# Optimization experiments

Hardware: AMD Instinct MI355X
Metric: run time of the kernel (lower is better)

Reference implementation:

```python
import jax, jax.numpy as jnp
import numpy as np

B, S, D, O, E = 8, 4096, 1024, 1024, 64

def setup_inputs() -> dict:
    key = jax.random.key(0)
    kx, kgw, kgb, kew, keb = jax.random.split(key, 5)
    x = jax.random.normal(kx, (B, S, D), dtype=jnp.float32)
    gate_w = jax.random.normal(kgw, (E, D), dtype=jnp.float32) * 0.02
    gate_b = jnp.zeros((E,), dtype=jnp.float32)
    expert_w = jax.random.normal(kew, (E, D, O), dtype=jnp.float32) * 0.02
    expert_b = jnp.zeros((E, O), dtype=jnp.float32)
    return {"x": x, "gate_w": gate_w, "gate_b": gate_b,
            "expert_w": expert_w, "expert_b": expert_b}

def reference(x, gate_w, gate_b, expert_w, expert_b):
    # x: [B,S,D] -> flatten tokens. With world_size=1 the all-reduce and
    # all-to-alls in the torch module are identities, and per-chunk processing
    # is token-independent, so one global pass is mathematically identical.
    b, s, d = x.shape
    xt = x.reshape(-1, d)                                   # [N, D]
    logits = xt @ gate_w.T + gate_b                         # [N, E]
    gates = jax.nn.softmax(logits, axis=-1)
    sel = jnp.argmax(gates, axis=-1)                        # [N] top-1 expert
    order = jnp.argsort(sel)                                # stable sort by expert
    xs = xt[order]                                          # tokens grouped by expert
    counts = jnp.bincount(sel, length=E).astype(jnp.int32)  # tokens per expert
    # Grouped expert GEMM: row block e of xs multiplies expert_w[e].
    ys = jax.lax.ragged_dot(xs, expert_w, counts)           # [N, O]
    ys = ys + expert_b[sel[order]]
    # Combine: scatter sorted outputs back to original token positions.
    # (Note: torch output is NOT scaled by gate probability.)
    out = jnp.zeros((xt.shape[0], expert_w.shape[-1]), dtype=ys.dtype)
    out = out.at[order].set(ys)
    return out.reshape(b, s, -1)
```

## Files before the change

### kernel.cpp

```cpp
#include <hip/hip_runtime.h>
#include <hip/hip_bf16.h>

#define N_TOK 32768
#define DIM 1024
#define OUTD 1024
#define NEXP 64

typedef __attribute__((ext_vector_type(4))) float f32x4;
typedef __attribute__((ext_vector_type(8))) short bf16x8;

__device__ __forceinline__ unsigned short f2bf(float f) {
    unsigned int u = __builtin_bit_cast(unsigned int, f);
    u += 0x7FFFu + ((u >> 16) & 1u);
    return (unsigned short)(u >> 16);
}

#define GLOAD16(gp, lp) \
    __builtin_amdgcn_global_load_lds((const __attribute__((address_space(1))) void*)(gp), \
                                     (__attribute__((address_space(3))) void*)(lp), 16, 0, 0)

__global__ __launch_bounds__(256) void prep_kernel(const float* __restrict__ x,
        const float* __restrict__ gw, const float* __restrict__ gb,
        const float* __restrict__ ew,
        int* __restrict__ sel, int* __restrict__ nflag, int* __restrict__ flags,
        unsigned short* __restrict__ xb, unsigned short* __restrict__ wt)
{
    __shared__ __align__(16) char smem[18432];
    int tid = threadIdx.x;

    if (blockIdx.x < 512) {
        float (*xs)[36]  = (float(*)[36])smem;
        float (*wsm)[36] = (float(*)[36])(smem + 9216);
        int t0 = blockIdx.x * 64;
        int tg = tid >> 4, eg = tid & 15;

        float acc[4][4];
#pragma unroll
        for (int i = 0; i < 4; i++)
#pragma unroll
            for (int j = 0; j < 4; j++) acc[i][j] = 0.f;

        for (int k0 = 0; k0 < DIM; k0 += 32) {
            __syncthreads();
#pragma unroll
            for (int q = 0; q < 2; q++) {
                int cidx = tid + q * 256;
                int r = cidx >> 3, c4 = (cidx & 7) * 4;
                *reinterpret_cast<float4*>(&xs[r][c4]) =
                    *reinterpret_cast<const float4*>(&x[(size_t)(t0 + r) * DIM + k0 + c4]);
                *reinterpret_cast<float4*>(&wsm[r][c4]) =
                    *reinterpret_cast<const float4*>(&gw[(size_t)r * DIM + k0 + c4]);
            }
            __syncthreads();
            if (xb) {
                int r = tid >> 2, cc = (tid & 3) * 8;
                float4 v0 = *reinterpret_cast<const float4*>(&xs[r][cc]);
                float4 v1 = *reinterpret_cast<const float4*>(&xs[r][cc + 4]);
                uint4 p;
                p.x = (unsigned int)f2bf(v0.x) | ((unsigned int)f2bf(v0.y) << 16);
                p.y = (unsigned int)f2bf(v0.z) | ((unsigned int)f2bf(v0.w) << 16);
                p.z = (unsigned int)f2bf(v1.x) | ((unsigned int)f2bf(v1.y) << 16);
                p.w = (unsigned int)f2bf(v1.z) | ((unsigned int)f2bf(v1.w) << 16);
                *reinterpret_cast<uint4*>(&xb[(size_t)(t0 + r) * DIM + k0 + cc]) = p;
            }
#pragma unroll
            for (int kk4 = 0; kk4 < 8; kk4++) {
                float4 xv[4], wv[4];
#pragma unroll
                for (int i = 0; i < 4; i++)
                    xv[i] = *reinterpret_cast<const float4*>(&xs[tg + 16 * i][kk4 * 4]);
#pragma unroll
                for (int j = 0; j < 4; j++)
                    wv[j] = *reinterpret_cast<const float4*>(&wsm[eg + 16 * j][kk4 * 4]);
#pragma unroll
                for (int i = 0; i < 4; i++)
#pragma unroll
                    for (int j = 0; j < 4; j++) {
                        acc[i][j] = fmaf(xv[i].x, wv[j].x, acc[i][j]);
                        acc[i][j] = fmaf(xv[i].y, wv[j].y, acc[i][j]);
                        acc[i][j] = fmaf(xv[i].z, wv[j].z, acc[i][j]);
                        acc[i][j] = fmaf(xv[i].w, wv[j].w, acc[i][j]);
                    }
            }
        }
#pragma unroll
        for (int j = 0; j < 4; j++) {
            float b = gb[eg + 16 * j];
#pragma unroll
            for (int i = 0; i < 4; i++) acc[i][j] += b;
        }
#pragma unroll
        for (int i = 0; i < 4; i++) {
            float m1 = -1e30f, m2 = -1e30f; int e1 = 0;
#pragma unroll
            for (int j = 0; j < 4; j++) {
                float v = acc[i][j]; int e = eg + 16 * j;
                if (v > m1) { m2 = m1; m1 = v; e1 = e; }
                else if (v > m2) m2 = v;
            }
#pragma unroll
            for (int d = 1; d < 16; d <<= 1) {
                float om1 = __shfl_xor(m1, d, 16);
                float om2 = __shfl_xor(m2, d, 16);
                int   oe1 = __shfl_xor(e1, d, 16);
                if (om1 > m1 || (om1 == m1 && oe1 < e1)) {
                    m2 = fmaxf(om2, m1); m1 = om1; e1 = oe1;
                } else {
                    m2 = fmaxf(m2, om1);
                }
            }
            if (eg == 0) {
                int t = t0 + tg + 16 * i;
                sel[t] = e1;
                if (m1 - m2 < 1e-3f) {
                    int idx = atomicAdd(nflag, 1);
                    if (idx < 4096) flags[idx] = t;
                }
            }
        }
    } else {
        if (!wt) return;
        unsigned short (*ts)[68] = (unsigned short(*)[68])smem;
        int lin = blockIdx.x - 512;
        int e = lin >> 8;
        int d0 = (lin & 15) * 64, o0 = ((lin >> 4) & 15) * 64;
        const float* src = ew + (size_t)e * (DIM * OUTD);
        int r = tid >> 4, c = (tid & 15) * 4;
#pragma unroll
        for (int i = 0; i < 4; i++) {
            int rr = r + i * 16;
            float4 v = *reinterpret_cast<const float4*>(&src[(size_t)(d0 + rr) * OUTD + o0 + c]);
            ushort4 u;
            u.x = f2bf(v.x); u.y = f2bf(v.y); u.z = f2bf(v.z); u.w = f2bf(v.w);
            *reinterpret_cast<ushort4*>(&ts[rr][c]) = u;
        }
        __syncthreads();
        unsigned short* dst = wt + (size_t)e * (DIM * OUTD);
        int dc = tid & 7;
#pragma unroll
        for (int i = 0; i < 2; i++) {
            int oo = (tid >> 3) + i * 32;
            uint4 p;
            p.x = (unsigned int)ts[dc*8+0][oo] | ((unsigned int)ts[dc*8+1][oo] << 16);
            p.y = (unsigned int)ts[dc*8+2][oo] | ((unsigned int)ts[dc*8+3][oo] << 16);
            p.z = (unsigned int)ts[dc*8+4][oo] | ((unsigned int)ts[dc*8+5][oo] << 16);
            p.w = (unsigned int)ts[dc*8+6][oo] | ((unsigned int)ts[dc*8+7][oo] << 16);
            *reinterpret_cast<uint4*>(&dst[(size_t)(o0 + oo) * DIM + d0 + dc * 8]) = p;
        }
    }
}

__global__ __launch_bounds__(64) void gate_fix_kernel(const float* __restrict__ x,
        const float* __restrict__ gw, const float* __restrict__ gb,
        int* __restrict__ sel, const int* __restrict__ nflag, const int* __restrict__ flags)
{
    int n = *nflag; if (n > 4096) n = 4096;
    int b = blockIdx.x;
    if (b >= n) return;
    int t = flags[b];
    int e = threadIdx.x;
    const float* xr = x + (size_t)t * DIM;
    const float* wr = gw + (size_t)e * DIM;
    double acc = (double)gb[e];
    for (int k = 0; k < DIM; k += 4) {
        acc += (double)xr[k]   * (double)wr[k];
        acc += (double)xr[k+1] * (double)wr[k+1];
        acc += (double)xr[k+2] * (double)wr[k+2];
        acc += (double)xr[k+3] * (double)wr[k+3];
    }
    double m1 = acc; int e1 = e;
#pragma unroll
    for (int d = 1; d < 64; d <<= 1) {
        double om1 = __shfl_xor(m1, d, 64);
        int   oe1  = __shfl_xor(e1, d, 64);
        if (om1 > m1 || (om1 == m1 && oe1 < e1)) { m1 = om1; e1 = oe1; }
    }
    if (e == 0) sel[t] = e1;
}

__global__ __launch_bounds__(256) void hist_kernel(const int* __restrict__ sel,
                                                   int* __restrict__ counts)
{
    __shared__ int h[NEXP];
    int tid = threadIdx.x;
    if (tid < NEXP) h[tid] = 0;
    __syncthreads();
    int t = blockIdx.x * 256 + tid;
    atomicAdd(&h[sel[t]], 1);
    __syncthreads();
    if (tid < NEXP && h[tid]) atomicAdd(&counts[tid], h[tid]);
}

__global__ void sched_kernel(const int* __restrict__ counts, int* __restrict__ offsets,
                             int* __restrict__ schedE, int* __restrict__ schedR,
                             int* __restrict__ totalRB)
{
    if (threadIdx.x != 0) return;
    int off = 0, rb = 0;
    for (int e = 0; e < NEXP; e++) {
        int c = counts[e];
        offsets[e] = off;
        int nb = (c + 127) >> 7;
        for (int b2 = 0; b2 < nb; b2++) { schedE[rb] = e; schedR[rb] = b2 * 128; rb++; }
        off += c;
    }
    offsets[NEXP] = off;
    *totalRB = rb;
}

__global__ __launch_bounds__(256) void scatter_kernel(const int* __restrict__ sel,
        const int* __restrict__ offsets, int* __restrict__ cursor, int* __restrict__ perm)
{
    int t = blockIdx.x * 256 + threadIdx.x;
    int e = sel[t];
    int pos = offsets[e] + atomicAdd(&cursor[e], 1);
    perm[pos] = t;
}

__global__ __launch_bounds__(256) void moe_gemm2(
        const unsigned short* __restrict__ xb, const unsigned short* __restrict__ wt,
        const float* __restrict__ eb,
        const int* __restrict__ perm, const int* __restrict__ offsets,
        const int* __restrict__ counts, const int* __restrict__ schedE,
        const int* __restrict__ schedR, const int* __restrict__ totalRB,
        float* __restrict__ out)
{
    int lin = blockIdx.x;
    int rb = lin >> 3, cb = lin & 7;
    if (rb >= *totalRB) return;
    int e = schedE[rb], r0 = schedR[rb];
    int cnt = counts[e], base = offsets[e];

    __shared__ __align__(16) unsigned short As[8192];
    __shared__ __align__(16) unsigned short Bs[8192];
    __shared__ int toks[128];

    int tid = threadIdx.x;
    if (tid < 128) {
        int r = r0 + tid;
        toks[tid] = (r < cnt) ? perm[base + r] : -1;
    }
    __syncthreads();

    int lane = tid & 63;
    int wv = tid >> 6;
    int wr = wv >> 1, wc = wv & 1;
    int lr = lane & 15, lg = lane >> 4;

    int rowS = tid >> 2;
    int koff = (((tid & 3) ^ ((tid >> 3) & 3)) * 8);
    int tokA1 = toks[rowS];      if (tokA1 < 0) tokA1 = 0;
    int tokA2 = toks[64 + rowS]; if (tokA2 < 0) tokA2 = 0;

    const unsigned short* wte = wt + ((size_t)e << 20);
    const unsigned short* bSrc1 = wte + (size_t)(cb * 128 + rowS) * DIM + koff;
    const unsigned short* bSrc2 = wte + (size_t)(cb * 128 + 64 + rowS) * DIM + koff;
    const unsigned short* aSrc1 = xb + (size_t)tokA1 * DIM + koff;
    const unsigned short* aSrc2 = xb + (size_t)tokA2 * DIM + koff;

    unsigned short* AsW0 = As + wv * 512;
    unsigned short* AsW1 = As + 2048 + wv * 512;
    unsigned short* BsW0 = Bs + wv * 512;
    unsigned short* BsW1 = Bs + 2048 + wv * 512;

    f32x4 acc[4][4];
#pragma unroll
    for (int m = 0; m < 4; m++)
#pragma unroll
        for (int n = 0; n < 4; n++)
#pragma unroll
            for (int c = 0; c < 4; c++) acc[m][n][c] = 0.f;

    const char* Asc = (const char*)As;
    const char* Bsc = (const char*)Bs;
    int fko = ((lg ^ ((lr >> 1) & 3)) * 16);

    auto stage = [&](int buf, int k0) {
        int off = buf * 4096;
        GLOAD16(bSrc1 + k0, BsW0 + off);
        GLOAD16(bSrc2 + k0, BsW1 + off);
        GLOAD16(aSrc1 + k0, AsW0 + off);
        GLOAD16(aSrc2 + k0, AsW1 + off);
    };
    auto compute = [&](int buf) {
        int boff = buf * 8192;
        bf16x8 bfr[4];
#pragma unroll
        for (int n = 0; n < 4; n++) {
            int row = wc * 64 + n * 16 + lr;
            bfr[n] = *reinterpret_cast<const bf16x8*>(Bsc + boff + (row << 6) + fko);
        }
#pragma unroll
        for (int m = 0; m < 4; m++) {
            int row = wr * 64 + m * 16 + lr;
            bf16x8 afr = *reinterpret_cast<const bf16x8*>(Asc + boff + (row << 6) + fko);
#pragma unroll
            for (int n = 0; n < 4; n++)
                acc[m][n] = __builtin_amdgcn_mfma_f32_16x16x32_bf16(afr, bfr[n], acc[m][n], 0, 0, 0);
        }
    };

    stage(0, 0);
    asm volatile("s_waitcnt vmcnt(0)" ::: "memory");
    __builtin_amdgcn_s_barrier();
    asm volatile("" ::: "memory");

    int cur = 0;
#pragma unroll 1
    for (int t = 0; t < 31; ++t) {
        stage(cur ^ 1, (t + 1) * 32);
        compute(cur);
        asm volatile("s_waitcnt vmcnt(0)" ::: "memory");
        __builtin_amdgcn_s_barrier();
        asm volatile("" ::: "memory");
        cur ^= 1;
    }
    compute(cur);

#pragma unroll
    for (int n = 0; n < 4; n++) {
        int oc = cb * 128 + wc * 64 + n * 16 + lr;
        float bias = eb[e * OUTD + oc];
#pragma unroll
        for (int m = 0; m < 4; m++) {
#pragma unroll
            for (int i2 = 0; i2 < 4; i2++) {
                int rr = wr * 64 + m * 16 + lg * 4 + i2;
                int tk = toks[rr];
                if (tk >= 0)
                    out[(size_t)tk * OUTD + oc] = acc[m][n][i2] + bias;
            }
        }
    }
}

__global__ __launch_bounds__(256) void moe_gemm_legacy(const float* __restrict__ x,
        const float* __restrict__ ew, const float* __restrict__ eb,
        const int* __restrict__ perm, const int* __restrict__ offsets,
        const int* __restrict__ counts, const int* __restrict__ schedE,
        const int* __restrict__ schedR, const int* __restrict__ totalRB,
        float* __restrict__ out)
{
    int rb = blockIdx.x;
    if (rb >= *totalRB) return;
    int cb = blockIdx.y;
    int e = schedE[rb], r0 = schedR[rb];
    int cnt = counts[e], base = offsets[e];

    __shared__ __align__(16) unsigned short As[128][40];
    __shared__ __align__(16) unsigned short Bs[128][40];
    __shared__ int toks[128];

    int tid = threadIdx.x;
    if (tid < 128) {
        int r = r0 + tid;
        toks[tid] = (r < cnt) ? perm[base + r] : -1;
    }
    __syncthreads();

    int lane = tid & 63;
    int wave = tid >> 6;
    int wr = wave >> 1, wc = wave & 1;
    int lr = lane & 15, lg = lane >> 4;

    f32x4 acc[4][4];
#pragma unroll
    for (int m = 0; m < 4; m++)
#pragma unroll
        for (int n = 0; n < 4; n++)
#pragma unroll
            for (int c = 0; c < 4; c++) acc[m][n][c] = 0.f;

    int aRow[4]; int aTok[4];
#pragma unroll
    for (int q = 0; q < 4; q++) {
        aRow[q] = (tid >> 3) + q * 32;
        int tk = toks[aRow[q]];
        aTok[q] = (tk < 0) ? 0 : tk;
    }
    int ac4 = tid & 7;
    int d0 = (tid >> 5) * 4;
    int o_lane = tid & 31;
    const float* wb = ew + (size_t)e * (DIM * OUTD) + (size_t)cb * 128;

    for (int k0 = 0; k0 < DIM; k0 += 32) {
        float4 av[4];
#pragma unroll
        for (int q = 0; q < 4; q++)
            av[q] = *reinterpret_cast<const float4*>(&x[(size_t)aTok[q] * DIM + k0 + ac4 * 4]);
        float bv[4][4];
#pragma unroll
        for (int i2 = 0; i2 < 4; i2++)
#pragma unroll
            for (int j = 0; j < 4; j++)
                bv[i2][j] = wb[(size_t)(k0 + d0 + i2) * OUTD + o_lane + 32 * j];

        __syncthreads();
#pragma unroll
        for (int q = 0; q < 4; q++) {
            uint2 p;
            p.x = (unsigned int)f2bf(av[q].x) | ((unsigned int)f2bf(av[q].y) << 16);
            p.y = (unsigned int)f2bf(av[q].z) | ((unsigned int)f2bf(av[q].w) << 16);
            *reinterpret_cast<uint2*>(&As[aRow[q]][ac4 * 4]) = p;
        }
#pragma unroll
        for (int j = 0; j < 4; j++) {
            uint2 p;
            p.x = (unsigned int)f2bf(bv[0][j]) | ((unsigned int)f2bf(bv[1][j]) << 16);
            p.y = (unsigned int)f2bf(bv[2][j]) | ((unsigned int)f2bf(bv[3][j]) << 16);
            *reinterpret_cast<uint2*>(&Bs[o_lane + 32 * j][d0]) = p;
        }
        __syncthreads();

        bf16x8 bfr[4];
#pragma unroll
        for (int n = 0; n < 4; n++)
            bfr[n] = *reinterpret_cast<const bf16x8*>(&Bs[wc * 64 + n * 16 + lr][lg * 8]);
#pragma unroll
        for (int m = 0; m < 4; m++) {
            bf16x8 afr = *reinterpret_cast<const bf16x8*>(&As[wr * 64 + m * 16 + lr][lg * 8]);
#pragma unroll
            for (int n = 0; n < 4; n++)
                acc[m][n] = __builtin_amdgcn_mfma_f32_16x16x32_bf16(afr, bfr[n], acc[m][n], 0, 0, 0);
        }
    }

#pragma unroll
    for (int n = 0; n < 4; n++) {
        int oc = cb * 128 + wc * 64 + n * 16 + lr;
        float bias = eb[e * OUTD + oc];
#pragma unroll
        for (int m = 0; m < 4; m++) {
#pragma unroll
            for (int i2 = 0; i2 < 4; i2++) {
                int rr = wr * 64 + m * 16 + lg * 4 + i2;
                int tk = toks[rr];
                if (tk >= 0)
                    out[(size_t)tk * OUTD + oc] = acc[m][n][i2] + bias;
            }
        }
    }
}

extern "C" void kernel_launch(void* const* d_in, const int* in_sizes, int n_in,
                              void* d_out, int out_size, void* d_ws, size_t ws_size,
                              hipStream_t stream)
{
    const float* x  = (const float*)d_in[0];
    const float* gw = (const float*)d_in[1];
    const float* gb = (const float*)d_in[2];
    const float* ew = (const float*)d_in[3];
    const float* eb = (const float*)d_in[4];
    float* out = (float*)d_out;

    char* ws = (char*)d_ws;
    int* counts  = (int*)(ws + 0);
    int* cursor  = (int*)(ws + 256);
    int* offsets = (int*)(ws + 512);
    int* totalRB = (int*)(ws + 1024);
    int* nflag   = (int*)(ws + 1028);
    int* flags   = (int*)(ws + 1032);
    int* schedE  = (int*)(ws + 20480);
    int* schedR  = (int*)(ws + 22528);
    int* sel     = (int*)(ws + 24576);
    int* perm    = (int*)(ws + 155648);

    const size_t WT_OFF   = (size_t)1 << 20;
    const size_t WT_BYTES = (size_t)NEXP * DIM * OUTD * 2;
    const size_t XB_OFF   = WT_OFF + WT_BYTES;
    const size_t XB_BYTES = (size_t)N_TOK * DIM * 2;
    int mode = (ws_size >= XB_OFF + XB_BYTES) ? 2
             : (ws_size >= WT_OFF + WT_BYTES) ? 1 : 0;
    unsigned short* wt = (mode >= 1) ? (unsigned short*)(ws + WT_OFF) : nullptr;
    unsigned short* xb = (mode == 2) ? (unsigned short*)(ws + XB_OFF) : nullptr;

    hipMemsetAsync(ws, 0, 2048, stream);

    prep_kernel<<<dim3(512 + ((mode >= 1) ? 16384 : 0)), 256, 0, stream>>>(
        x, gw, gb, ew, sel, nflag, flags, xb, wt);
    gate_fix_kernel<<<dim3(4096), 64, 0, stream>>>(x, gw, gb, sel, nflag, flags);
    hist_kernel<<<dim3(N_TOK / 256), 256, 0, stream>>>(sel, counts);
    sched_kernel<<<dim3(1), 64, 0, stream>>>(counts, offsets, schedE, schedR, totalRB);
    scatter_kernel<<<dim3(N_TOK / 256), 256, 0, stream>>>(sel, offsets, cursor, perm);

    if (mode == 2)
        moe_gemm2<<<dim3(2560), 256, 0, stream>>>(xb, wt, eb, perm, offsets, counts,
                                                  schedE, schedR, totalRB, out);
    else
        moe_gemm_legacy<<<dim3(320, 8), 256, 0, stream>>>(x, ew, eb, perm, offsets, counts,
                                                          schedE, schedR, totalRB, out);
}
```

Baseline: 445.8 us.

## Enlarge expert GEMM tile to 256x256, fuse histogram into gating, parallelize scheduling

The grouped expert GEMM moves from 128x128 tiles with 256 threads to 256x256 tiles with 512 threads (8 waves, 128x64 per wave). It also gets an XCD-aware block-to-tile mapping, so each weight and activation tile is reused across more MFMA work. The separate histogram kernel is removed: per-expert counts are now gathered with global atomics in the gating kernel and patched in gate_fix when a near-tie token changes expert. The single-thread scheduler becomes a wave-wide prefix scan. The cost is a larger accumulator footprint with register-pressure risk under launch_bounds(512,2), more padding waste on partial row blocks, and contended global atomics on 64 counters.

```diff
diff --git a/kernel.cpp b/kernel.cpp
--- a/kernel.cpp
+++ b/kernel.cpp
@@ -23,6 +23,7 @@
         const float* __restrict__ gw, const float* __restrict__ gb,
         const float* __restrict__ ew,
         int* __restrict__ sel, int* __restrict__ nflag, int* __restrict__ flags,
+        int* __restrict__ counts,
         unsigned short* __restrict__ xb, unsigned short* __restrict__ wt)
 {
     __shared__ __align__(16) char smem[18432];
@@ -112,6 +113,7 @@
             if (eg == 0) {
                 int t = t0 + tg + 16 * i;
                 sel[t] = e1;
+                atomicAdd(&counts[e1], 1);
                 if (m1 - m2 < 1e-3f) {
                     int idx = atomicAdd(nflag, 1);
                     if (idx < 4096) flags[idx] = t;
@@ -152,7 +154,8 @@
 
 __global__ __launch_bounds__(64) void gate_fix_kernel(const float* __restrict__ x,
         const float* __restrict__ gw, const float* __restrict__ gb,
-        int* __restrict__ sel, const int* __restrict__ nflag, const int* __restrict__ flags)
+        int* __restrict__ sel, const int* __restrict__ nflag, const int* __restrict__ flags,
+        int* __restrict__ counts)
 {
     int n = *nflag; if (n > 4096) n = 4096;
     int b = blockIdx.x;
@@ -175,37 +178,35 @@
         int   oe1  = __shfl_xor(e1, d, 64);
         if (om1 > m1 || (om1 == m1 && oe1 < e1)) { m1 = om1; e1 = oe1; }
     }
-    if (e == 0) sel[t] = e1;
-}
-
-__global__ __launch_bounds__(256) void hist_kernel(const int* __restrict__ sel,
-                                                   int* __restrict__ counts)
-{
-    __shared__ int h[NEXP];
-    int tid = threadIdx.x;
-    if (tid < NEXP) h[tid] = 0;
-    __syncthreads();
-    int t = blockIdx.x * 256 + tid;
-    atomicAdd(&h[sel[t]], 1);
-    __syncthreads();
-    if (tid < NEXP && h[tid]) atomicAdd(&counts[tid], h[tid]);
+    if (e == 0) {
+        int eOld = sel[t];
+        if (eOld != e1) {
+            sel[t] = e1;
+            atomicSub(&counts[eOld], 1);
+            atomicAdd(&counts[e1], 1);
+        }
+    }
 }
 
 __global__ void sched_kernel(const int* __restrict__ counts, int* __restrict__ offsets,
                              int* __restrict__ schedE, int* __restrict__ schedR,
-                             int* __restrict__ totalRB)
-{
-    if (threadIdx.x != 0) return;
-    int off = 0, rb = 0;
-    for (int e = 0; e < NEXP; e++) {
-        int c = counts[e];
-        offsets[e] = off;
-        int nb = (c + 127) >> 7;
-        for (int b2 = 0; b2 < nb; b2++) { schedE[rb] = e; schedR[rb] = b2 * 128; rb++; }
-        off += c;
-    }
-    offsets[NEXP] = off;
-    *totalRB = rb;
+                             int* __restrict__ totalRB, int rowsShift)
+{
+    int e = threadIdx.x;
+    int c = counts[e];
+    int v = c;
+#pragma unroll
+    for (int d = 1; d < 64; d <<= 1) { int y = __shfl_up(v, d, 64); if (e >= d) v += y; }
+    offsets[e] = v - c;
+    if (e == 63) offsets[NEXP] = v;
+    int rows = 1 << rowsShift;
+    int nb = (c + rows - 1) >> rowsShift;
+    int rbv = nb;
+#pragma unroll
+    for (int d = 1; d < 64; d <<= 1) { int y = __shfl_up(rbv, d, 64); if (e >= d) rbv += y; }
+    int rbBase = rbv - nb;
+    for (int i = 0; i < nb; i++) { schedE[rbBase + i] = e; schedR[rbBase + i] = i << rowsShift; }
+    if (e == 63) *totalRB = rbv;
 }
 
 __global__ __launch_bounds__(256) void scatter_kernel(const int* __restrict__ sel,
@@ -217,7 +218,7 @@
     perm[pos] = t;
 }
 
-__global__ __launch_bounds__(256) void moe_gemm2(
+__global__ __launch_bounds__(512, 2) void moe_gemm3(
         const unsigned short* __restrict__ xb, const unsigned short* __restrict__ wt,
         const float* __restrict__ eb,
         const int* __restrict__ perm, const int* __restrict__ offsets,
@@ -225,18 +226,20 @@
         const int* __restrict__ schedR, const int* __restrict__ totalRB,
         float* __restrict__ out)
 {
-    int lin = blockIdx.x;
-    int rb = lin >> 3, cb = lin & 7;
+    int xcd = blockIdx.x & 7;
+    int slot = blockIdx.x >> 3;
+    int rb = slot * 2 + (xcd >> 2);
+    int cb = xcd & 3;
     if (rb >= *totalRB) return;
     int e = schedE[rb], r0 = schedR[rb];
     int cnt = counts[e], base = offsets[e];
 
-    __shared__ __align__(16) unsigned short As[8192];
-    __shared__ __align__(16) unsigned short Bs[8192];
-    __shared__ int toks[128];
+    __shared__ __align__(16) unsigned short As[16384];
+    __shared__ __align__(16) unsigned short Bs[16384];
+    __shared__ int toks[256];
 
     int tid = threadIdx.x;
-    if (tid < 128) {
+    if (tid < 256) {
         int r = r0 + tid;
         toks[tid] = (r < cnt) ? perm[base + r] : -1;
     }
@@ -244,28 +247,28 @@
 
     int lane = tid & 63;
     int wv = tid >> 6;
-    int wr = wv >> 1, wc = wv & 1;
+    int wr = wv >> 2, wc = wv & 3;
     int lr = lane & 15, lg = lane >> 4;
 
     int rowS = tid >> 2;
-    int koff = (((tid & 3) ^ ((tid >> 3) & 3)) * 8);
-    int tokA1 = toks[rowS];      if (tokA1 < 0) tokA1 = 0;
-    int tokA2 = toks[64 + rowS]; if (tokA2 < 0) tokA2 = 0;
+    int koff = ((tid & 3) ^ ((tid >> 3) & 3)) * 8;
+    int tokA1 = toks[rowS];       if (tokA1 < 0) tokA1 = 0;
+    int tokA2 = toks[128 + rowS]; if (tokA2 < 0) tokA2 = 0;
 
     const unsigned short* wte = wt + ((size_t)e << 20);
-    const unsigned short* bSrc1 = wte + (size_t)(cb * 128 + rowS) * DIM + koff;
-    const unsigned short* bSrc2 = wte + (size_t)(cb * 128 + 64 + rowS) * DIM + koff;
     const unsigned short* aSrc1 = xb + (size_t)tokA1 * DIM + koff;
     const unsigned short* aSrc2 = xb + (size_t)tokA2 * DIM + koff;
-
-    unsigned short* AsW0 = As + wv * 512;
-    unsigned short* AsW1 = As + 2048 + wv * 512;
-    unsigned short* BsW0 = Bs + wv * 512;
-    unsigned short* BsW1 = Bs + 2048 + wv * 512;
-
-    f32x4 acc[4][4];
-#pragma unroll
-    for (int m = 0; m < 4; m++)
+    const unsigned short* bSrc1 = wte + (size_t)(cb * 256 + rowS) * DIM + koff;
+    const unsigned short* bSrc2 = wte + (size_t)(cb * 256 + 128 + rowS) * DIM + koff;
+
+    unsigned short* AsQ0 = As + wv * 512;
+    unsigned short* AsQ1 = As + 4096 + wv * 512;
+    unsigned short* BsQ0 = Bs + wv * 512;
+    unsigned short* BsQ1 = Bs + 4096 + wv * 512;
+
+    f32x4 acc[8][4];
+#pragma unroll
+    for (int m = 0; m < 8; m++)
 #pragma unroll
         for (int n = 0; n < 4; n++)
 #pragma unroll
@@ -273,17 +276,17 @@
 
     const char* Asc = (const char*)As;
     const char* Bsc = (const char*)Bs;
-    int fko = ((lg ^ ((lr >> 1) & 3)) * 16);
+    int fko = (lg ^ ((lr >> 1) & 3)) * 16;
 
     auto stage = [&](int buf, int k0) {
-        int off = buf * 4096;
-        GLOAD16(bSrc1 + k0, BsW0 + off);
-        GLOAD16(bSrc2 + k0, BsW1 + off);
-        GLOAD16(aSrc1 + k0, AsW0 + off);
-        GLOAD16(aSrc2 + k0, AsW1 + off);
+        int off = buf * 8192;
+        GLOAD16(bSrc1 + k0, BsQ0 + off);
+        GLOAD16(bSrc2 + k0, BsQ1 + off);
+        GLOAD16(aSrc1 + k0, AsQ0 + off);
+        GLOAD16(aSrc2 + k0, AsQ1 + off);
     };
     auto compute = [&](int buf) {
-        int boff = buf * 8192;
+        int boff = buf * 16384;
         bf16x8 bfr[4];
 #pragma unroll
         for (int n = 0; n < 4; n++) {
@@ -291,8 +294,8 @@
             bfr[n] = *reinterpret_cast<const bf16x8*>(Bsc + boff + (row << 6) + fko);
         }
 #pragma unroll
-        for (int m = 0; m < 4; m++) {
-            int row = wr * 64 + m * 16 + lr;
+        for (int m = 0; m < 8; m++) {
+            int row = wr * 128 + m * 16 + lr;
             bf16x8 afr = *reinterpret_cast<const bf16x8*>(Asc + boff + (row << 6) + fko);
 #pragma unroll
             for (int n = 0; n < 4; n++)
@@ -319,13 +322,13 @@
 
 #pragma unroll
     for (int n = 0; n < 4; n++) {
-        int oc = cb * 128 + wc * 64 + n * 16 + lr;
+        int oc = cb * 256 + wc * 64 + n * 16 + lr;
         float bias = eb[e * OUTD + oc];
 #pragma unroll
-        for (int m = 0; m < 4; m++) {
+        for (int m = 0; m < 8; m++) {
 #pragma unroll
             for (int i2 = 0; i2 < 4; i2++) {
-                int rr = wr * 64 + m * 16 + lg * 4 + i2;
+                int rr = wr * 128 + m * 16 + lg * 4 + i2;
                 int tk = toks[rr];
                 if (tk >= 0)
                     out[(size_t)tk * OUTD + oc] = acc[m][n][i2] + bias;
@@ -469,23 +472,22 @@
     const size_t WT_BYTES = (size_t)NEXP * DIM * OUTD * 2;
     const size_t XB_OFF   = WT_OFF + WT_BYTES;
     const size_t XB_BYTES = (size_t)N_TOK * DIM * 2;
-    int mode = (ws_size >= XB_OFF + XB_BYTES) ? 2
-             : (ws_size >= WT_OFF + WT_BYTES) ? 1 : 0;
-    unsigned short* wt = (mode >= 1) ? (unsigned short*)(ws + WT_OFF) : nullptr;
+    int mode = (ws_size >= XB_OFF + XB_BYTES) ? 2 : 0;
+    unsigned short* wt = (mode == 2) ? (unsigned short*)(ws + WT_OFF) : nullptr;
     unsigned short* xb = (mode == 2) ? (unsigned short*)(ws + XB_OFF) : nullptr;
 
     hipMemsetAsync(ws, 0, 2048, stream);
 
-    prep_kernel<<<dim3(512 + ((mode >= 1) ? 16384 : 0)), 256, 0, stream>>>(
-        x, gw, gb, ew, sel, nflag, flags, xb, wt);
-    gate_fix_kernel<<<dim3(4096), 64, 0, stream>>>(x, gw, gb, sel, nflag, flags);
-    hist_kernel<<<dim3(N_TOK / 256), 256, 0, stream>>>(sel, counts);
-    sched_kernel<<<dim3(1), 64, 0, stream>>>(counts, offsets, schedE, schedR, totalRB);
+    prep_kernel<<<dim3(512 + ((mode == 2) ? 16384 : 0)), 256, 0, stream>>>(
+        x, gw, gb, ew, sel, nflag, flags, counts, xb, wt);
+    gate_fix_kernel<<<dim3(4096), 64, 0, stream>>>(x, gw, gb, sel, nflag, flags, counts);
+    sched_kernel<<<dim3(1), 64, 0, stream>>>(counts, offsets, schedE, schedR, totalRB,
+                                             (mode == 2) ? 8 : 7);
     scatter_kernel<<<dim3(N_TOK / 256), 256, 0, stream>>>(sel, offsets, cursor, perm);
 
     if (mode == 2)
-        moe_gemm2<<<dim3(2560), 256, 0, stream>>>(xb, wt, eb, perm, offsets, counts,
-                                                  schedE, schedR, totalRB, out);
+        moe_gemm3<<<dim3(768), 512, 0, stream>>>(xb, wt, eb, perm, offsets, counts,
+                                                 schedE, schedR, totalRB, out);
     else
         moe_gemm_legacy<<<dim3(320, 8), 256, 0, stream>>>(x, ew, eb, perm, offsets, counts,
                                                           schedE, schedR, totalRB, out);
```

New measurement: 523.4 us. 1.17x slower.
